# Performance work log

Measured on AMD Instinct MI355X. Metric: run time of the kernel, lower is better.

## Reference

```python
import jax, jax.numpy as jnp
import numpy as np

GAMMA = 1.0


def setup_inputs() -> dict:
    key = jax.random.key(0)
    k1, k2, k3 = jax.random.split(key, 3)
    n_query, n_train, d = 8192, 8192, 512
    X = jax.random.normal(k1, (n_query, d), dtype=jnp.float32)
    train_X = jax.random.normal(k2, (n_train, d), dtype=jnp.float32)
    dual_coef = jax.random.normal(k3, (n_train,), dtype=jnp.float32)
    return {"X": X, "train_X": train_X, "dual_coef": dual_coef}


def _rbf_kernel(x, y, gamma):
    x2 = jnp.sum(x * x, axis=-1, keepdims=True)          # (n_x, 1)
    y2 = jnp.sum(y * y, axis=-1)[None, :]                # (1, n_y)
    sq_dist = x2 + y2 - 2.0 * jnp.einsum('qd,td->qt', x, y)
    sq_dist = jnp.maximum(sq_dist, 0.0)                  # guard tiny negatives
    return jnp.exp(-gamma * sq_dist)                     # (n_x, n_y)


def reference(X, train_X, dual_coef):
    K_test = _rbf_kernel(X, train_X, GAMMA)              # (n_query, n_train)
    return K_test @ dual_coef                            # (n_query,)
```

## Files before the change

### kernel.cpp

```cpp
#include <hip/hip_runtime.h>
#include <hip/hip_bf16.h>
#include <stdint.h>

#define NQ 8192
#define NT 8192
#define DIM 512
#define BK 64
#define NKT (DIM / BK)
#define BM 256
#define BN 256
#define AELEMS (BM * BK)
#define BUF_ELEMS ((BM + BN) * BK)

typedef __hip_bfloat16 bf16;
using bf16x8  = __attribute__((ext_vector_type(8))) short;
using f32x4   = __attribute__((ext_vector_type(4))) float;
using short8v = __attribute__((ext_vector_type(8))) short;

typedef __attribute__((address_space(1))) void* gas1_t;
typedef __attribute__((address_space(3))) void* las3_t;

__global__ void zero_out_k(float* __restrict__ out) {
    out[blockIdx.x * 256 + threadIdx.x] = 0.0f;
}

__global__ void prep_k(const float* __restrict__ X, const float* __restrict__ T,
                       bf16* __restrict__ Xb, bf16* __restrict__ Tb,
                       float* __restrict__ x2, float* __restrict__ y2) {
    const int w    = threadIdx.x >> 6;
    const int lane = threadIdx.x & 63;
    const int wid  = blockIdx.x * 4 + w;
#pragma unroll
    for (int rr = 0; rr < 2; ++rr) {
        const int row = wid * 2 + rr;
        const float* src; bf16* dst; float* nrm; int r;
        if (row < NQ) { r = row;      src = X + (size_t)r * DIM; dst = Xb + (size_t)r * DIM; nrm = x2; }
        else          { r = row - NQ; src = T + (size_t)r * DIM; dst = Tb + (size_t)r * DIM; nrm = y2; }
        const float4 v0 = reinterpret_cast<const float4*>(src)[lane * 2];
        const float4 v1 = reinterpret_cast<const float4*>(src)[lane * 2 + 1];
        float s = v0.x*v0.x + v0.y*v0.y + v0.z*v0.z + v0.w*v0.w
                + v1.x*v1.x + v1.y*v1.y + v1.z*v1.z + v1.w*v1.w;
        short8v pk;
        pk[0] = (short)__bfloat16_as_ushort(__float2bfloat16(v0.x));
        pk[1] = (short)__bfloat16_as_ushort(__float2bfloat16(v0.y));
        pk[2] = (short)__bfloat16_as_ushort(__float2bfloat16(v0.z));
        pk[3] = (short)__bfloat16_as_ushort(__float2bfloat16(v0.w));
        pk[4] = (short)__bfloat16_as_ushort(__float2bfloat16(v1.x));
        pk[5] = (short)__bfloat16_as_ushort(__float2bfloat16(v1.y));
        pk[6] = (short)__bfloat16_as_ushort(__float2bfloat16(v1.z));
        pk[7] = (short)__bfloat16_as_ushort(__float2bfloat16(v1.w));
        reinterpret_cast<short8v*>(dst)[lane] = pk;
#pragma unroll
        for (int off = 32; off; off >>= 1) s += __shfl_xor(s, off, 64);
        if (lane == 0) nrm[r] = s;
    }
}

__device__ __forceinline__ void stage_rows(
    const bf16* __restrict__ src, int rowBase, int kt, bf16* dst, int w, int lane) {
    const int k0 = kt * BK;
    const int rl = lane >> 3;
    const int c  = (lane & 7) ^ rl;
#pragma unroll
    for (int j = 0; j < 4; ++j) {
        const int R0 = w * 32 + j * 8;
        const bf16* g = src + (size_t)(rowBase + R0 + rl) * DIM + k0 + c * 8;
        __builtin_amdgcn_global_load_lds((gas1_t)g, (las3_t)(dst + R0 * BK), 16, 0, 0);
    }
}

__device__ __forceinline__ bf16x8 frag(const bf16* base, int row, int kc) {
    return *reinterpret_cast<const bf16x8*>(
        base + row * BK + ((kc ^ (row & 7)) << 3));
}

#define MFMA16(A, B, C) __builtin_amdgcn_mfma_f32_16x16x32_bf16(A, B, C, 0, 0, 0)

template<bool ST, bool LAST>
__device__ __forceinline__ void ktile(
    const bf16* __restrict__ Tb, const bf16* __restrict__ Xb,
    int tBlk, int qBlk, int tS, const bf16* bufC, bf16* bufS,
    int wm, int wn, int w, int lane, f32x4 (&acc)[8][4]) {

    const bf16* cA = bufC;
    const bf16* cB = bufC + AELEMS;
    const int fr = lane & 15;
    const int fc = lane >> 4;

    if (ST) {
        stage_rows(Tb, tBlk, tS, bufS, w, lane);
        stage_rows(Xb, qBlk, tS, bufS + AELEMS, w, lane);
    }
#pragma unroll
    for (int kh = 0; kh < 2; ++kh) {
        const int kc = kh * 4 + fc;
        bf16x8 a[8], b[4];
#pragma unroll
        for (int m = 0; m < 8; ++m) a[m] = frag(cA, wm * 128 + m * 16 + fr, kc);
#pragma unroll
        for (int n = 0; n < 4; ++n) b[n] = frag(cB, wn * 64 + n * 16 + fr, kc);
        __builtin_amdgcn_s_setprio(1);
#pragma unroll
        for (int m = 0; m < 8; ++m)
#pragma unroll
            for (int n = 0; n < 4; ++n)
                acc[m][n] = MFMA16(a[m], b[n], acc[m][n]);
        __builtin_amdgcn_s_setprio(0);
    }
    if (!LAST) {
        asm volatile("s_waitcnt vmcnt(0)" ::: "memory");
        __builtin_amdgcn_s_barrier();
        __builtin_amdgcn_sched_barrier(0);
    }
}

__global__ __launch_bounds__(512, 2) void krr_mfma_k(
    const bf16* __restrict__ Tb, const bf16* __restrict__ Xb,
    const float* __restrict__ x2, const float* __restrict__ y2,
    const float* __restrict__ coef, float* __restrict__ out) {

    __shared__ bf16 lds[2 * BUF_ELEMS];

    const int tid  = threadIdx.x;
    const int w    = tid >> 6;
    const int lane = tid & 63;
    const int wm   = w >> 2;
    const int wn   = w & 3;

    const int qBlk = blockIdx.x * BN;
    const int tBlk = blockIdx.y * BM;

    f32x4 acc[8][4];
    const f32x4 z4 = {0.f, 0.f, 0.f, 0.f};
#pragma unroll
    for (int m = 0; m < 8; ++m)
#pragma unroll
        for (int n = 0; n < 4; ++n) acc[m][n] = z4;

    stage_rows(Tb, tBlk, 0, lds, w, lane);
    stage_rows(Xb, qBlk, 0, lds + AELEMS, w, lane);
    asm volatile("s_waitcnt vmcnt(0)" ::: "memory");
    __builtin_amdgcn_s_barrier();
    __builtin_amdgcn_sched_barrier(0);

#pragma unroll 1
    for (int t = 0; t < NKT - 1; ++t) {
        const bf16* bufC = lds + (t & 1) * BUF_ELEMS;
        bf16* bufS       = lds + ((t + 1) & 1) * BUF_ELEMS;
        ktile<true, false>(Tb, Xb, tBlk, qBlk, t + 1, bufC, bufS, wm, wn, w, lane, acc);
    }
    ktile<false, true>(Tb, Xb, tBlk, qBlk, 0,
                       lds + ((NKT - 1) & 1) * BUF_ELEMS, lds, wm, wn, w, lane, acc);

    float s[4], x2q[4];
#pragma unroll
    for (int n = 0; n < 4; ++n) {
        s[n]   = 0.f;
        x2q[n] = x2[qBlk + wn * 64 + n * 16 + (lane & 15)];
    }
#pragma unroll
    for (int m = 0; m < 8; ++m) {
        const int tb = tBlk + wm * 128 + m * 16 + ((lane >> 4) << 2);
        float y2v[4], cfv[4];
#pragma unroll
        for (int r = 0; r < 4; ++r) { y2v[r] = y2[tb + r]; cfv[r] = coef[tb + r]; }
#pragma unroll
        for (int n = 0; n < 4; ++n)
#pragma unroll
            for (int r = 0; r < 4; ++r) {
                const float d  = acc[m][n][r];
                const float sq = fmaxf(x2q[n] + y2v[r] - 2.0f * d, 0.f);
                s[n] += __expf(-sq) * cfv[r];
            }
    }
#pragma unroll
    for (int n = 0; n < 4; ++n) {
        float v = s[n];
        v += __shfl_xor(v, 16, 64);
        v += __shfl_xor(v, 32, 64);
        if (lane < 16) atomicAdd(&out[qBlk + wn * 64 + n * 16 + lane], v);
    }
}

__global__ void krr_naive_k(const float* __restrict__ X, const float* __restrict__ T,
                            const float* __restrict__ coef, float* __restrict__ out) {
    __shared__ float xq[DIM];
    const int q = blockIdx.x;
    for (int i = threadIdx.x; i < DIM; i += 256) xq[i] = X[(size_t)q * DIM + i];
    __syncthreads();
    float s2 = 0.f;
    for (int i = 0; i < DIM; ++i) s2 += xq[i] * xq[i];
    float acc = 0.f;
    for (int t = threadIdx.x; t < NT; t += 256) {
        const float* ty = T + (size_t)t * DIM;
        float dot = 0.f, yy = 0.f;
        for (int i = 0; i < DIM; ++i) { float yv = ty[i]; dot += xq[i] * yv; yy += yv * yv; }
        float sq = fmaxf(s2 + yy - 2.0f * dot, 0.f);
        acc += __expf(-sq) * coef[t];
    }
#pragma unroll
    for (int off = 32; off > 0; off >>= 1) acc += __shfl_down(acc, off, 64);
    __shared__ float red[4];
    if ((threadIdx.x & 63) == 0) red[threadIdx.x >> 6] = acc;
    __syncthreads();
    if (threadIdx.x == 0) out[q] = red[0] + red[1] + red[2] + red[3];
}

extern "C" void kernel_launch(void* const* d_in, const int* in_sizes, int n_in,
                              void* d_out, int out_size, void* d_ws, size_t ws_size,
                              hipStream_t stream) {
    const float* X    = (const float*)d_in[0];
    const float* T    = (const float*)d_in[1];
    const float* coef = (const float*)d_in[2];
    float* out = (float*)d_out;

    zero_out_k<<<NQ / 256, 256, 0, stream>>>(out);

    const size_t need = (size_t)(NQ + NT) * DIM * sizeof(bf16) + (size_t)(NQ + NT) * sizeof(float);
    if (ws_size >= need) {
        bf16* Xb  = (bf16*)d_ws;
        bf16* Tb  = Xb + (size_t)NQ * DIM;
        float* x2 = (float*)(Tb + (size_t)NT * DIM);
        float* y2 = x2 + NQ;
        prep_k<<<2048, 256, 0, stream>>>(X, T, Xb, Tb, x2, y2);
        dim3 grid(NQ / BN, NT / BM);
        krr_mfma_k<<<grid, 512, 0, stream>>>(Tb, Xb, x2, y2, coef, out);
    } else {
        krr_naive_k<<<NQ, 256, 0, stream>>>(X, T, coef, out);
    }
}
```

Before: 146.5 us.

## Switch distance GEMM from bf16 to fp8 scaled MFMA 16x16x128

Operands are now quantized to FP8 in the prep kernel instead of bf16. The main kernel stages 128-byte K tiles and issues the gfx950 scaled f8f6f4 MFMA with unit scales, one instruction per 128-wide K step. This halves the bytes moved through global memory and LDS and doubles MFMA throughput. The cost is much lower precision in the dot products: errors of order 0.1 or more are amplified through exp(-dist) on large distances, which risks failing the accuracy tolerance.

```diff
diff --git a/kernel.cpp b/kernel.cpp
--- a/kernel.cpp
+++ b/kernel.cpp
@@ -5,17 +5,16 @@
 #define NQ 8192
 #define NT 8192
 #define DIM 512
-#define BK 64
-#define NKT (DIM / BK)
+#define BKB 128
+#define NKT (DIM / BKB)
 #define BM 256
 #define BN 256
-#define AELEMS (BM * BK)
-#define BUF_ELEMS ((BM + BN) * BK)
-
-typedef __hip_bfloat16 bf16;
-using bf16x8  = __attribute__((ext_vector_type(8))) short;
-using f32x4   = __attribute__((ext_vector_type(4))) float;
-using short8v = __attribute__((ext_vector_type(8))) short;
+#define ABYTES (BM * BKB)
+#define BUFB ((BM + BN) * BKB)
+
+using f32x4  = __attribute__((ext_vector_type(4))) float;
+using i32x4  = __attribute__((ext_vector_type(4))) int;
+using i32x8  = __attribute__((ext_vector_type(8))) int;
 
 typedef __attribute__((address_space(1))) void* gas1_t;
 typedef __attribute__((address_space(3))) void* las3_t;
@@ -25,7 +24,7 @@
 }
 
 __global__ void prep_k(const float* __restrict__ X, const float* __restrict__ T,
-                       bf16* __restrict__ Xb, bf16* __restrict__ Tb,
+                       uint8_t* __restrict__ Xb, uint8_t* __restrict__ Tb,
                        float* __restrict__ x2, float* __restrict__ y2) {
     const int w    = threadIdx.x >> 6;
     const int lane = threadIdx.x & 63;
@@ -33,23 +32,18 @@
 #pragma unroll
     for (int rr = 0; rr < 2; ++rr) {
         const int row = wid * 2 + rr;
-        const float* src; bf16* dst; float* nrm; int r;
+        const float* src; uint8_t* dst; float* nrm; int r;
         if (row < NQ) { r = row;      src = X + (size_t)r * DIM; dst = Xb + (size_t)r * DIM; nrm = x2; }
         else          { r = row - NQ; src = T + (size_t)r * DIM; dst = Tb + (size_t)r * DIM; nrm = y2; }
         const float4 v0 = reinterpret_cast<const float4*>(src)[lane * 2];
         const float4 v1 = reinterpret_cast<const float4*>(src)[lane * 2 + 1];
         float s = v0.x*v0.x + v0.y*v0.y + v0.z*v0.z + v0.w*v0.w
                 + v1.x*v1.x + v1.y*v1.y + v1.z*v1.z + v1.w*v1.w;
-        short8v pk;
-        pk[0] = (short)__bfloat16_as_ushort(__float2bfloat16(v0.x));
-        pk[1] = (short)__bfloat16_as_ushort(__float2bfloat16(v0.y));
-        pk[2] = (short)__bfloat16_as_ushort(__float2bfloat16(v0.z));
-        pk[3] = (short)__bfloat16_as_ushort(__float2bfloat16(v0.w));
-        pk[4] = (short)__bfloat16_as_ushort(__float2bfloat16(v1.x));
-        pk[5] = (short)__bfloat16_as_ushort(__float2bfloat16(v1.y));
-        pk[6] = (short)__bfloat16_as_ushort(__float2bfloat16(v1.z));
-        pk[7] = (short)__bfloat16_as_ushort(__float2bfloat16(v1.w));
-        reinterpret_cast<short8v*>(dst)[lane] = pk;
+        int lo = __builtin_amdgcn_cvt_pk_fp8_f32(v0.x, v0.y, 0, false);
+        lo     = __builtin_amdgcn_cvt_pk_fp8_f32(v0.z, v0.w, lo, true);
+        int hi = __builtin_amdgcn_cvt_pk_fp8_f32(v1.x, v1.y, 0, false);
+        hi     = __builtin_amdgcn_cvt_pk_fp8_f32(v1.z, v1.w, hi, true);
+        reinterpret_cast<int2*>(dst)[lane] = make_int2(lo, hi);
 #pragma unroll
         for (int off = 32; off; off >>= 1) s += __shfl_xor(s, off, 64);
         if (lane == 0) nrm[r] = s;
@@ -57,56 +51,58 @@
 }
 
 __device__ __forceinline__ void stage_rows(
-    const bf16* __restrict__ src, int rowBase, int kt, bf16* dst, int w, int lane) {
-    const int k0 = kt * BK;
+    const uint8_t* __restrict__ src, int rowBase, int kt, uint8_t* dst, int w, int lane) {
+    const int k0 = kt * BKB;
     const int rl = lane >> 3;
     const int c  = (lane & 7) ^ rl;
 #pragma unroll
     for (int j = 0; j < 4; ++j) {
         const int R0 = w * 32 + j * 8;
-        const bf16* g = src + (size_t)(rowBase + R0 + rl) * DIM + k0 + c * 8;
-        __builtin_amdgcn_global_load_lds((gas1_t)g, (las3_t)(dst + R0 * BK), 16, 0, 0);
-    }
-}
-
-__device__ __forceinline__ bf16x8 frag(const bf16* base, int row, int kc) {
-    return *reinterpret_cast<const bf16x8*>(
-        base + row * BK + ((kc ^ (row & 7)) << 3));
-}
-
-#define MFMA16(A, B, C) __builtin_amdgcn_mfma_f32_16x16x32_bf16(A, B, C, 0, 0, 0)
+        const uint8_t* g = src + (size_t)(rowBase + R0 + rl) * DIM + k0 + c * 16;
+        __builtin_amdgcn_global_load_lds((gas1_t)g, (las3_t)(dst + R0 * BKB), 16, 0, 0);
+    }
+}
+
+__device__ __forceinline__ i32x8 frag8(const uint8_t* base, int row, int fc) {
+    const uint8_t* p = base + row * BKB;
+    const i32x4 lo = *reinterpret_cast<const i32x4*>(p + ((( 2 * fc )     ^ (row & 7)) << 4));
+    const i32x4 hi = *reinterpret_cast<const i32x4*>(p + (((2 * fc + 1) ^ (row & 7)) << 4));
+    i32x8 r = { lo[0], lo[1], lo[2], lo[3], hi[0], hi[1], hi[2], hi[3] };
+    return r;
+}
+
+#define MFMA_FP8(A, B, C)                                               \
+    __builtin_amdgcn_mfma_scale_f32_16x16x128_f8f6f4(                   \
+        (A), (B), (C), 0 , 0 ,                \
+        0, 0x7F7F7F7F, 0, 0x7F7F7F7F)
 
 template<bool ST, bool LAST>
 __device__ __forceinline__ void ktile(
-    const bf16* __restrict__ Tb, const bf16* __restrict__ Xb,
-    int tBlk, int qBlk, int tS, const bf16* bufC, bf16* bufS,
+    const uint8_t* __restrict__ Tb, const uint8_t* __restrict__ Xb,
+    int tBlk, int qBlk, int tS, const uint8_t* bufC, uint8_t* bufS,
     int wm, int wn, int w, int lane, f32x4 (&acc)[8][4]) {
 
-    const bf16* cA = bufC;
-    const bf16* cB = bufC + AELEMS;
+    const uint8_t* cA = bufC;
+    const uint8_t* cB = bufC + ABYTES;
     const int fr = lane & 15;
     const int fc = lane >> 4;
 
     if (ST) {
         stage_rows(Tb, tBlk, tS, bufS, w, lane);
-        stage_rows(Xb, qBlk, tS, bufS + AELEMS, w, lane);
-    }
-#pragma unroll
-    for (int kh = 0; kh < 2; ++kh) {
-        const int kc = kh * 4 + fc;
-        bf16x8 a[8], b[4];
-#pragma unroll
-        for (int m = 0; m < 8; ++m) a[m] = frag(cA, wm * 128 + m * 16 + fr, kc);
-#pragma unroll
-        for (int n = 0; n < 4; ++n) b[n] = frag(cB, wn * 64 + n * 16 + fr, kc);
-        __builtin_amdgcn_s_setprio(1);
-#pragma unroll
-        for (int m = 0; m < 8; ++m)
-#pragma unroll
-            for (int n = 0; n < 4; ++n)
-                acc[m][n] = MFMA16(a[m], b[n], acc[m][n]);
-        __builtin_amdgcn_s_setprio(0);
-    }
+        stage_rows(Xb, qBlk, tS, bufS + ABYTES, w, lane);
+    }
+    i32x8 a[8], b[4];
+#pragma unroll
+    for (int m = 0; m < 8; ++m) a[m] = frag8(cA, wm * 128 + m * 16 + fr, fc);
+#pragma unroll
+    for (int n = 0; n < 4; ++n) b[n] = frag8(cB, wn * 64 + n * 16 + fr, fc);
+    __builtin_amdgcn_s_setprio(1);
+#pragma unroll
+    for (int m = 0; m < 8; ++m)
+#pragma unroll
+        for (int n = 0; n < 4; ++n)
+            acc[m][n] = MFMA_FP8(a[m], b[n], acc[m][n]);
+    __builtin_amdgcn_s_setprio(0);
     if (!LAST) {
         asm volatile("s_waitcnt vmcnt(0)" ::: "memory");
         __builtin_amdgcn_s_barrier();
@@ -115,11 +111,11 @@
 }
 
 __global__ __launch_bounds__(512, 2) void krr_mfma_k(
-    const bf16* __restrict__ Tb, const bf16* __restrict__ Xb,
+    const uint8_t* __restrict__ Tb, const uint8_t* __restrict__ Xb,
     const float* __restrict__ x2, const float* __restrict__ y2,
     const float* __restrict__ coef, float* __restrict__ out) {
 
-    __shared__ bf16 lds[2 * BUF_ELEMS];
+    __shared__ uint8_t lds[2 * BUFB];
 
     const int tid  = threadIdx.x;
     const int w    = tid >> 6;
@@ -138,19 +134,19 @@
         for (int n = 0; n < 4; ++n) acc[m][n] = z4;
 
     stage_rows(Tb, tBlk, 0, lds, w, lane);
-    stage_rows(Xb, qBlk, 0, lds + AELEMS, w, lane);
+    stage_rows(Xb, qBlk, 0, lds + ABYTES, w, lane);
     asm volatile("s_waitcnt vmcnt(0)" ::: "memory");
     __builtin_amdgcn_s_barrier();
     __builtin_amdgcn_sched_barrier(0);
 
 #pragma unroll 1
     for (int t = 0; t < NKT - 1; ++t) {
-        const bf16* bufC = lds + (t & 1) * BUF_ELEMS;
-        bf16* bufS       = lds + ((t + 1) & 1) * BUF_ELEMS;
+        const uint8_t* bufC = lds + (t & 1) * BUFB;
+        uint8_t* bufS       = lds + ((t + 1) & 1) * BUFB;
         ktile<true, false>(Tb, Xb, tBlk, qBlk, t + 1, bufC, bufS, wm, wn, w, lane, acc);
     }
     ktile<false, true>(Tb, Xb, tBlk, qBlk, 0,
-                       lds + ((NKT - 1) & 1) * BUF_ELEMS, lds, wm, wn, w, lane, acc);
+                       lds + ((NKT - 1) & 1) * BUFB, lds, wm, wn, w, lane, acc);
 
     float s[4], x2q[4];
 #pragma unroll
@@ -216,12 +212,12 @@
 
     zero_out_k<<<NQ / 256, 256, 0, stream>>>(out);
 
-    const size_t need = (size_t)(NQ + NT) * DIM * sizeof(bf16) + (size_t)(NQ + NT) * sizeof(float);
+    const size_t need = (size_t)(NQ + NT) * DIM + (size_t)(NQ + NT) * sizeof(float);
     if (ws_size >= need) {
-        bf16* Xb  = (bf16*)d_ws;
-        bf16* Tb  = Xb + (size_t)NQ * DIM;
-        float* x2 = (float*)(Tb + (size_t)NT * DIM);
-        float* y2 = x2 + NQ;
+        uint8_t* Xb = (uint8_t*)d_ws;
+        uint8_t* Tb = Xb + (size_t)NQ * DIM;
+        float* x2   = (float*)(Tb + (size_t)NT * DIM);
+        float* y2   = x2 + NQ;
         prep_k<<<2048, 256, 0, stream>>>(X, T, Xb, Tb, x2, y2);
         dim3 grid(NQ / BN, NT / BM);
         krr_mfma_k<<<grid, 512, 0, stream>>>(Tb, Xb, x2, y2, coef, out);
```

Measured after the change: 145.9 us. No clear change (-0.4%).
